# Optimization experiments

Hardware: AMD Instinct MI355X
Metric: run time of the kernel (lower is better)

## Reference

```python
import jax, jax.numpy as jnp
import numpy as np

B, T, A, F, K, DQ, DV = 64, 1024, 128, 1024, 31, 1024, 512  # filters F == T required by source math


def setup_inputs() -> dict:
    key = jax.random.key(0)
    ks = jax.random.split(key, 8)
    s = 0.05
    return {
        "query": jax.random.normal(ks[0], (B, 1, DQ), jnp.float32),
        "value": jax.random.normal(ks[1], (B, T, DV), jnp.float32),
        "attention_weights_cat": jax.random.uniform(ks[2], (B, T, 2), jnp.float32),
        "Wq": jax.random.normal(ks[3], (DQ, A), jnp.float32) * s,
        "Wm": jax.random.normal(ks[4], (DV, A), jnp.float32) * s,
        "Wv": jax.random.normal(ks[5], (A, 1), jnp.float32) * s,
        "Wconv": jax.random.normal(ks[6], (K, 2, F), jnp.float32) * s,
        "Wloc": jax.random.normal(ks[7], (T, A), jnp.float32) * s,
    }


def reference(query, value, attention_weights_cat, Wq, Wm, Wv, Wconv, Wloc):
    # query_layer: Dense(tanh, no bias): [B,1,DQ] -> [B,1,A]
    q = jnp.tanh(jnp.einsum('bld,da->bla', query, Wq))
    # memory_layer: Dense(tanh, no bias): [B,T,DV] -> [B,T,A]
    v = jnp.tanh(jnp.einsum('btd,da->bta', value, Wm))
    # location conv (SAME, no bias): [B,T,2] -> [B,T,F]
    loc = jax.lax.conv_general_dilated(
        attention_weights_cat, Wconv, window_strides=(1,), padding='SAME',
        dimension_numbers=('NWC', 'WIO', 'NWC'))
    # source transposes [0,2,1] then Dense(T->A, tanh): [B,F,T] -> [B,F,A]
    loc = jnp.tanh(jnp.einsum('bft,ta->bfa', jnp.transpose(loc, (0, 2, 1)), Wloc))
    # additive score (F == T so broadcast add is element-aligned): [B,T,1]
    score = jnp.einsum('bta,ao->bto', jnp.tanh(q + v + loc), Wv)
    alignment = jax.nn.softmax(score, axis=1)                # softmax over time
    context = jnp.sum(alignment * v, axis=1)                  # [B,A]
    return context, jnp.transpose(alignment, (0, 2, 1))       # [B,1,T]
```

## Files before the change

### kernel.cpp

```cpp
#include <hip/hip_runtime.h>
#include <hip/hip_bf16.h>

#define BB 64
#define TT 1024
#define AA 128
#define FF 1024
#define DQ 1024
#define DV 512

typedef __bf16 bf16x8_t __attribute__((ext_vector_type(8)));
typedef __bf16 bf16x4_t __attribute__((ext_vector_type(4)));
typedef float f32x4_t __attribute__((ext_vector_type(4)));
typedef _Float16 f16x4_t __attribute__((ext_vector_type(4)));

__device__ __forceinline__ float ftanh(float x) {
    float e = __expf(2.0f * x);
    return 1.0f - 2.0f / (e + 1.0f);
}

__device__ __forceinline__ __bf16 bhi(float x) { return (__bf16)x; }
__device__ __forceinline__ __bf16 blo(float x) {
    __bf16 h = (__bf16)x;
    return (__bf16)(x - (float)h);
}

__global__ __launch_bounds__(256) void k_prep(
    const float* __restrict__ Wm, const float* __restrict__ Wconv,
    const float* __restrict__ Wloc, const float* __restrict__ query,
    const float* __restrict__ Wq,
    __bf16* __restrict__ pwmhi, __bf16* __restrict__ pwmlo,
    __bf16* __restrict__ wcthi, __bf16* __restrict__ wctlo,
    __bf16* __restrict__ pwlhi, __bf16* __restrict__ pwllo,
    float* __restrict__ q_ws) {
    __shared__ float ls[128 * 65];
    int bx = blockIdx.x, tid = threadIdx.x;
    if (bx < 16) {
        int s = bx, d0 = s * 32;
        for (int i = tid; i < 4096; i += 256) {
            int dd = i >> 7, a = i & 127;
            ls[a * 33 + dd] = Wm[(d0 + dd) * AA + a];
        }
        __syncthreads();
#pragma unroll
        for (int u = 0; u < 2; u++) {
            int pos = tid * 2 + u;
            int l15 = pos & 15, lq = (pos >> 4) & 3, g = pos >> 6;
            bf16x8_t h8, l8;
#pragma unroll
            for (int j = 0; j < 8; j++) {
                float x = ls[(g * 16 + l15) * 33 + lq * 8 + j];
                h8[j] = bhi(x);
                l8[j] = blo(x);
            }
            size_t off = (size_t)(s * 512 + pos) * 8;
            *(bf16x8_t*)(pwmhi + off) = h8;
            *(bf16x8_t*)(pwmlo + off) = l8;
        }
    } else if (bx < 24) {
        int f0 = (bx - 16) * 128;
        for (int i = tid; i < 8192; i += 256) {
            int kc = i >> 7, f = i & 127;
            ls[f * 65 + kc] = (kc < 62) ? Wconv[kc * FF + f0 + f] : 0.f;
        }
        __syncthreads();
        int f = tid >> 1, half = tid & 1;
#pragma unroll
        for (int g = 0; g < 4; g++) {
            bf16x8_t h8, l8;
#pragma unroll
            for (int j = 0; j < 8; j++) {
                float x = ls[f * 65 + half * 32 + g * 8 + j];
                h8[j] = bhi(x);
                l8[j] = blo(x);
            }
            size_t off = (size_t)(f0 + f) * 64 + half * 32 + g * 8;
            *(bf16x8_t*)(wcthi + off) = h8;
            *(bf16x8_t*)(wctlo + off) = l8;
        }
    } else if (bx < 56) {
        int s2 = bx - 24, t0 = s2 * 32;
        for (int i = tid; i < 4096; i += 256) {
            int tt = i >> 7, a = i & 127;
            ls[a * 33 + tt] = Wloc[(t0 + tt) * AA + a];
        }
        __syncthreads();
#pragma unroll
        for (int u = 0; u < 2; u++) {
            int pos = tid * 2 + u;
            int l15 = pos & 15, lq = (pos >> 4) & 3, g = pos >> 6;
            bf16x8_t h8, l8;
#pragma unroll
            for (int j = 0; j < 8; j++) {
                float x = ls[(g * 16 + l15) * 33 + lq * 8 + j];
                h8[j] = bhi(x);
                l8[j] = blo(x);
            }
            size_t off = (size_t)(s2 * 512 + pos) * 8;
            *(bf16x8_t*)(pwlhi + off) = h8;
            *(bf16x8_t*)(pwllo + off) = l8;
        }
    } else {
        int b = bx - 56;
        int a = tid & 127, half = tid >> 7;
        const float* qrow = query + b * DQ + half * 512;
        float a0 = 0.f, a1 = 0.f, a2 = 0.f, a3 = 0.f;
        for (int d = 0; d < 512; d += 4) {
            float4 qv = *(const float4*)(qrow + d);
            int dg = (half * 512 + d) * AA + a;
            a0 += qv.x * Wq[dg];
            a1 += qv.y * Wq[dg + AA];
            a2 += qv.z * Wq[dg + 2 * AA];
            a3 += qv.w * Wq[dg + 3 * AA];
        }
        ls[tid] = a0 + a1 + a2 + a3;
        __syncthreads();
        if (half == 0) q_ws[b * AA + a] = ftanh(ls[a] + ls[a + 128]);
    }
}

__global__ __launch_bounds__(256) void k_zq(
    const float* __restrict__ xcat,
    const __bf16* __restrict__ pwlhi, const __bf16* __restrict__ pwllo,
    float* __restrict__ ztf) {
    int bx = blockIdx.x;
    int b = bx & 63, ahh = (bx >> 6) & 1, kh = bx >> 7;
    int tid = threadIdx.x;
    __shared__ float xs0[1056], xs1[1056];
    __shared__ float zs[64 * 66];
    for (int i = tid; i < 1056; i += 256) {
        int t = i - 16;
        float2 xv = (t >= 0 && t < TT) ? *(const float2*)(xcat + (size_t)(b * TT + t) * 2)
                                       : make_float2(0.f, 0.f);
        xs0[i] = xv.x;
        xs1[i] = xv.y;
    }
    __syncthreads();
    int lane = tid & 63, wid = tid >> 6;
    int wm = wid >> 1, wn = wid & 1;
    int l15 = lane & 15, lq = lane >> 4;

    f32x4_t zacc[2][2];
#pragma unroll
    for (int mi = 0; mi < 2; mi++)
#pragma unroll
        for (int ni = 0; ni < 2; ni++) zacc[mi][ni] = (f32x4_t){0.f, 0.f, 0.f, 0.f};

    int phase = bx & 15;
    for (int sl = 0; sl < 16; sl++) {
        int s = kh * 16 + ((sl + phase) & 15);
        int t0 = s * 32;
        bf16x8_t bh[2], bl[2];
#pragma unroll
        for (int ni = 0; ni < 2; ni++) {
            int g = ahh * 4 + wn * 2 + ni;
            size_t poff = (size_t)((s * 8 + g) * 64 + lane) * 8;
            bh[ni] = *(const bf16x8_t*)(pwlhi + poff);
            bl[ni] = *(const bf16x8_t*)(pwllo + poff);
        }
        bf16x8_t ah_[2], al_[2];
#pragma unroll
        for (int mi = 0; mi < 2; mi++) {
            int kc = wm * 32 + mi * 16 + l15;
            const float* xsc = (kc & 1) ? xs1 : xs0;
            int base = t0 + lq * 8 + (kc >> 1) + 1;
#pragma unroll
            for (int j = 0; j < 8; j++) {
                float x = xsc[base + j];
                ah_[mi][j] = bhi(x);
                al_[mi][j] = blo(x);
            }
        }
#pragma unroll
        for (int ni = 0; ni < 2; ni++)
#pragma unroll
            for (int mi = 0; mi < 2; mi++) {
                zacc[mi][ni] = __builtin_amdgcn_mfma_f32_16x16x32_bf16(ah_[mi], bh[ni], zacc[mi][ni], 0, 0, 0);
                zacc[mi][ni] = __builtin_amdgcn_mfma_f32_16x16x32_bf16(al_[mi], bh[ni], zacc[mi][ni], 0, 0, 0);
                zacc[mi][ni] = __builtin_amdgcn_mfma_f32_16x16x32_bf16(ah_[mi], bl[ni], zacc[mi][ni], 0, 0, 0);
            }
    }
#pragma unroll
    for (int mi = 0; mi < 2; mi++)
#pragma unroll
        for (int ni = 0; ni < 2; ni++)
#pragma unroll
            for (int r = 0; r < 4; r++)
                zs[(wm * 32 + mi * 16 + lq * 4 + r) * 66 + wn * 32 + ni * 16 + l15] = zacc[mi][ni][r];
    __syncthreads();
    int a_local = tid & 63, seg = tid >> 6;
#pragma unroll
    for (int g = 0; g < 2; g++) {
        f32x4_t v0, v1;
#pragma unroll
        for (int j = 0; j < 4; j++) {
            v0[j] = zs[(seg * 16 + g * 8 + j) * 66 + a_local];
            v1[j] = zs[(seg * 16 + g * 8 + 4 + j) * 66 + a_local];
        }
        float* dst = ztf + (size_t)kh * 524288 +
                     ((size_t)b * AA + ahh * 64 + a_local) * 64 + seg * 16 + g * 8;
        *(f32x4_t*)dst = v0;
        *(f32x4_t*)(dst + 4) = v1;
    }
}

__global__ __launch_bounds__(256, 2) void k_main(
    const float* __restrict__ value,
    const __bf16* __restrict__ pwmhi, const __bf16* __restrict__ pwmlo,
    const __bf16* __restrict__ wcthi, const __bf16* __restrict__ wctlo,
    const float* __restrict__ ztf,
    const float* __restrict__ q_ws, const float* __restrict__ Wv,
    _Float16* __restrict__ v_ws, float* __restrict__ score) {
    int b = blockIdx.x >> 3;
    int trow0 = (blockIdx.x & 7) << 7;
    int tid = threadIdx.x;
    int lane = tid & 63, wid = tid >> 6;
    int wm = wid >> 1, wn = wid & 1;
    int l15 = lane & 15, lq = lane >> 4;
    int phase = (blockIdx.x + (blockIdx.x >> 3)) & 15;

    __shared__ __align__(16) float As[2][128 * 32];
    __shared__ float sc_red[256];

    f32x4_t acc[4][4];
#pragma unroll
    for (int mi = 0; mi < 4; mi++)
#pragma unroll
        for (int ni = 0; ni < 4; ni++) acc[mi][ni] = (f32x4_t){0.f, 0.f, 0.f, 0.f};

    int l3 = lane >> 3;
    int su = (lane & 7) ^ l3;
    const float* aG[4];
    unsigned aL[4];
#pragma unroll
    for (int i = 0; i < 4; i++) {
        int row = (wid * 4 + i) * 8 + l3;
        aG[i] = value + (size_t)(b * TT + trow0 + row) * DV + su * 4;
        aL[i] = (unsigned)((wid * 4 + i) * 1024);
    }
    const __bf16* pbh0 = pwmhi + (size_t)(wn * 256 + lane) * 8;
    const __bf16* pbl0 = pwmlo + (size_t)(wn * 256 + lane) * 8;

    bf16x8_t bhb[2][4], blb[2][4];

#define GL4(dst, ptr, OFF) \
    asm volatile("global_load_dwordx4 %0, %1, off offset:" OFF : "=v"(dst) : "v"(ptr))
#define ISSUE_B(bf, s) { \
    const __bf16* _bh = pbh0 + (size_t)(s) * 4096; \
    const __bf16* _bl = pbl0 + (size_t)(s) * 4096; \
    GL4(bhb[bf][0], _bh, "0"); \
    GL4(bhb[bf][1], _bh, "1024"); \
    GL4(bhb[bf][2], _bh, "2048"); \
    GL4(bhb[bf][3], _bh, "3072"); \
    GL4(blb[bf][0], _bl, "0"); \
    GL4(blb[bf][1], _bl, "1024"); \
    GL4(blb[bf][2], _bl, "2048"); \
    GL4(blb[bf][3], _bl, "3072"); }
#define STAGE_A(bf, s)                                                                      \
    {                                                                                       \
        _Pragma("unroll") for (int i = 0; i < 4; i++)                                       \
            __builtin_amdgcn_global_load_lds(                                               \
                (const __attribute__((address_space(1))) void*)(aG[i] + (s) * 32),          \
                (__attribute__((address_space(3))) void*)((char*)&As[bf][0] + aL[i]),       \
                16, 0, 0);                                                                  \
    }

    {
        int s0 = phase & 15;
        ISSUE_B(0, s0);
        STAGE_A(0, s0);
    }

    int swz = l15 & 7;
#pragma unroll
    for (int it = 0; it < 16; ++it) {
        const int cb = it & 1;
        __syncthreads();
        __builtin_amdgcn_sched_barrier(0);

        bf16x8_t ah[4], al[4];
#pragma unroll
        for (int mi = 0; mi < 4; mi++) {
            int row = wm * 64 + mi * 16 + l15;
            const char* rbase = (const char*)&As[cb][0] + row * 128;
            f32x4_t f0 = *(const f32x4_t*)(rbase + (((lq * 2 + 0) ^ swz) << 4));
            f32x4_t f1 = *(const f32x4_t*)(rbase + (((lq * 2 + 1) ^ swz) << 4));
#pragma unroll
            for (int j = 0; j < 4; j++) {
                ah[mi][j] = bhi(f0[j]);
                al[mi][j] = blo(f0[j]);
                ah[mi][4 + j] = bhi(f1[j]);
                al[mi][4 + j] = blo(f1[j]);
            }
        }
        if (it < 15) {
            const int s = (it + 1 + phase) & 15;
            ISSUE_B(cb ^ 1, s);
            STAGE_A(cb ^ 1, s);
        }
#pragma unroll
        for (int mi = 0; mi < 4; mi++)
#pragma unroll
            for (int ni = 0; ni < 4; ni++) {
                acc[mi][ni] = __builtin_amdgcn_mfma_f32_16x16x32_bf16(ah[mi], bhb[cb][ni], acc[mi][ni], 0, 0, 0);
                acc[mi][ni] = __builtin_amdgcn_mfma_f32_16x16x32_bf16(al[mi], bhb[cb][ni], acc[mi][ni], 0, 0, 0);
                acc[mi][ni] = __builtin_amdgcn_mfma_f32_16x16x32_bf16(ah[mi], blb[cb][ni], acc[mi][ni], 0, 0, 0);
            }
    }
#undef ISSUE_B
#undef STAGE_A
#undef GL4

    f32x4_t lacc[4][4];
#pragma unroll
    for (int mi = 0; mi < 4; mi++)
#pragma unroll
        for (int ni = 0; ni < 4; ni++) lacc[mi][ni] = (f32x4_t){0.f, 0.f, 0.f, 0.f};
#pragma unroll
    for (int kc0 = 0; kc0 < 64; kc0 += 32) {
        bf16x8_t a2h[4], a2l[4], b2h[4], b2l[4];
#pragma unroll
        for (int mi = 0; mi < 4; mi++) {
            int f = trow0 + wm * 64 + mi * 16 + l15;
            a2h[mi] = *(const bf16x8_t*)(wcthi + (size_t)f * 64 + kc0 + lq * 8);
            a2l[mi] = *(const bf16x8_t*)(wctlo + (size_t)f * 64 + kc0 + lq * 8);
        }
#pragma unroll
        for (int ni = 0; ni < 4; ni++) {
            int a = wn * 64 + ni * 16 + l15;
            const float* zp = ztf + ((size_t)b * AA + a) * 64 + kc0 + lq * 8;
            f32x4_t z0 = *(const f32x4_t*)zp + *(const f32x4_t*)(zp + 524288);
            f32x4_t z1 = *(const f32x4_t*)(zp + 4) + *(const f32x4_t*)(zp + 524292);
#pragma unroll
            for (int j = 0; j < 4; j++) {
                b2h[ni][j] = bhi(z0[j]);
                b2l[ni][j] = blo(z0[j]);
                b2h[ni][4 + j] = bhi(z1[j]);
                b2l[ni][4 + j] = blo(z1[j]);
            }
        }
#pragma unroll
        for (int mi = 0; mi < 4; mi++)
#pragma unroll
            for (int ni = 0; ni < 4; ni++) {
                lacc[mi][ni] = __builtin_amdgcn_mfma_f32_16x16x32_bf16(a2h[mi], b2h[ni], lacc[mi][ni], 0, 0, 0);
                lacc[mi][ni] = __builtin_amdgcn_mfma_f32_16x16x32_bf16(a2l[mi], b2h[ni], lacc[mi][ni], 0, 0, 0);
                lacc[mi][ni] = __builtin_amdgcn_mfma_f32_16x16x32_bf16(a2h[mi], b2l[ni], lacc[mi][ni], 0, 0, 0);
            }
    }

    float qv[4], wv[4];
#pragma unroll
    for (int ni = 0; ni < 4; ni++) {
        int a = wn * 64 + ni * 16 + l15;
        qv[ni] = q_ws[b * AA + a];
        wv[ni] = Wv[a];
    }
#pragma unroll
    for (int mi = 0; mi < 4; mi++) {
#pragma unroll
        for (int r = 0; r < 4; r++) {
            int tl = wm * 64 + mi * 16 + lq * 4 + r;
            int t = trow0 + tl;
            float s = 0.f;
#pragma unroll
            for (int ni = 0; ni < 4; ni++) {
                float v = ftanh(acc[mi][ni][r]);
                float loc = ftanh(lacc[mi][ni][r]);
                int a = wn * 64 + ni * 16 + l15;
                v_ws[(size_t)(b * TT + t) * AA + a] = (_Float16)v;
                s += ftanh(qv[ni] + v + loc) * wv[ni];
            }
            s += __shfl_xor(s, 1, 64);
            s += __shfl_xor(s, 2, 64);
            s += __shfl_xor(s, 4, 64);
            s += __shfl_xor(s, 8, 64);
            if (l15 == 0) sc_red[wn * 128 + tl] = s;
        }
    }
    __syncthreads();
    if (tid < 128) score[b * TT + trow0 + tid] = sc_red[tid] + sc_red[128 + tid];
}

__global__ void k_softmax(const float* __restrict__ score, float* __restrict__ out_align,
                          float* __restrict__ out_ctx) {
    int b = blockIdx.x, tid = threadIdx.x;
    if (tid < 128) out_ctx[b * AA + tid] = 0.f;
    __shared__ float red[4];
    float s[4];
#pragma unroll
    for (int i = 0; i < 4; i++) s[i] = score[b * TT + tid + i * 256];
    float m = fmaxf(fmaxf(s[0], s[1]), fmaxf(s[2], s[3]));
    for (int off = 32; off; off >>= 1) m = fmaxf(m, __shfl_xor(m, off, 64));
    int wid = tid >> 6;
    if ((tid & 63) == 0) red[wid] = m;
    __syncthreads();
    float M = fmaxf(fmaxf(red[0], red[1]), fmaxf(red[2], red[3]));
    __syncthreads();
    float e[4];
    float sum = 0.f;
#pragma unroll
    for (int i = 0; i < 4; i++) { e[i] = __expf(s[i] - M); sum += e[i]; }
    for (int off = 32; off; off >>= 1) sum += __shfl_xor(sum, off, 64);
    if ((tid & 63) == 0) red[wid] = sum;
    __syncthreads();
    float inv = 1.0f / (red[0] + red[1] + red[2] + red[3]);
#pragma unroll
    for (int i = 0; i < 4; i++) out_align[b * TT + tid + i * 256] = e[i] * inv;
}

__global__ void k_context(const float* __restrict__ align, const _Float16* __restrict__ v_ws,
                          float* __restrict__ out_ctx) {
    int b = blockIdx.y, t0 = blockIdx.x * 64, tid = threadIdx.x;
    int a0 = (tid & 31) * 4, tl = tid >> 5;
    __shared__ float sh[8 * 132];
    f32x4_t acc = (f32x4_t){0.f, 0.f, 0.f, 0.f};
    for (int tt = tl; tt < 64; tt += 8) {
        float w = align[b * TT + t0 + tt];
        f16x4_t vv = *(const f16x4_t*)(v_ws + (size_t)(b * TT + t0 + tt) * AA + a0);
        acc[0] += w * (float)vv[0];
        acc[1] += w * (float)vv[1];
        acc[2] += w * (float)vv[2];
        acc[3] += w * (float)vv[3];
    }
    *(f32x4_t*)&sh[tl * 132 + a0] = acc;
    __syncthreads();
    if (tid < 128) {
        float s = 0.f;
#pragma unroll
        for (int j = 0; j < 8; j++) s += sh[j * 132 + tid];
        atomicAdd(out_ctx + b * AA + tid, s);
    }
}

extern "C" void kernel_launch(void* const* d_in, const int* in_sizes, int n_in,
                              void* d_out, int out_size, void* d_ws, size_t ws_size,
                              hipStream_t stream) {
    const float* query = (const float*)d_in[0];
    const float* value = (const float*)d_in[1];
    const float* xcat  = (const float*)d_in[2];
    const float* Wq    = (const float*)d_in[3];
    const float* Wm    = (const float*)d_in[4];
    const float* Wv    = (const float*)d_in[5];
    const float* Wconv = (const float*)d_in[6];
    const float* Wloc  = (const float*)d_in[7];
    float* out = (float*)d_out;

    float* ws = (float*)d_ws;
    float* q_ws  = ws;
    float* sc_ws = q_ws + 8192;
    _Float16* v_ws = (_Float16*)(sc_ws + 65536);
    __bf16* pwmhi = (__bf16*)(sc_ws + 65536 + 4194304);
    __bf16* pwmlo = pwmhi + 65536;
    __bf16* wcthi = pwmlo + 65536;
    __bf16* wctlo = wcthi + 65536;
    __bf16* pwlhi = wctlo + 65536;
    __bf16* pwllo = pwlhi + 131072;
    float* ztf = (float*)(pwllo + 131072);

    k_prep<<<120, 256, 0, stream>>>(Wm, Wconv, Wloc, query, Wq,
                                    pwmhi, pwmlo, wcthi, wctlo, pwlhi, pwllo, q_ws);
    k_zq<<<256, 256, 0, stream>>>(xcat, pwlhi, pwllo, ztf);
    k_main<<<512, 256, 0, stream>>>(value, pwmhi, pwmlo, wcthi, wctlo, ztf,
                                    q_ws, Wv, v_ws, sc_ws);
    k_softmax<<<BB, 256, 0, stream>>>(sc_ws, out + 8192, out);
    k_context<<<dim3(16, BB), 256, 0, stream>>>(out + 8192, v_ws, out);
}
```

Measured before the change: 269.0 us.

## Stage Wm hi/lo tiles through LDS with async loads and explicit waitcnt

Replaces the per-wave register prefetch of the split bf16 Wm fragments with global_load_lds staging into double-buffered shared tiles, so each block fetches B once instead of each wave pair fetching its own copy. The loop now issues the next stage before compute, waits with an explicit vmcnt, and uses raw s_barrier plus a trailing barrier instead of __syncthreads. The main loop is no longer unrolled. This cuts redundant global traffic and VGPRs for B, but adds LDS reads and footprint (which may hurt occupancy) and depends on hand-counted waitcnt values being correct.

```diff
diff --git a/kernel.cpp b/kernel.cpp
--- a/kernel.cpp
+++ b/kernel.cpp
@@ -219,6 +219,8 @@
     int phase = (blockIdx.x + (blockIdx.x >> 3)) & 15;
 
     __shared__ __align__(16) float As[2][128 * 32];
+    __shared__ __align__(16) __bf16 Bh[2][512 * 8];
+    __shared__ __align__(16) __bf16 Bl[2][512 * 8];
     __shared__ float sc_red[256];
 
     f32x4_t acc[4][4];
@@ -237,44 +239,48 @@
         aG[i] = value + (size_t)(b * TT + trow0 + row) * DV + su * 4;
         aL[i] = (unsigned)((wid * 4 + i) * 1024);
     }
-    const __bf16* pbh0 = pwmhi + (size_t)(wn * 256 + lane) * 8;
-    const __bf16* pbl0 = pwmlo + (size_t)(wn * 256 + lane) * 8;
-
-    bf16x8_t bhb[2][4], blb[2][4];
-
-#define GL4(dst, ptr, OFF) \
-    asm volatile("global_load_dwordx4 %0, %1, off offset:" OFF : "=v"(dst) : "v"(ptr))
-#define ISSUE_B(bf, s) { \
-    const __bf16* _bh = pbh0 + (size_t)(s) * 4096; \
-    const __bf16* _bl = pbl0 + (size_t)(s) * 4096; \
-    GL4(bhb[bf][0], _bh, "0"); \
-    GL4(bhb[bf][1], _bh, "1024"); \
-    GL4(bhb[bf][2], _bh, "2048"); \
-    GL4(bhb[bf][3], _bh, "3072"); \
-    GL4(blb[bf][0], _bl, "0"); \
-    GL4(blb[bf][1], _bl, "1024"); \
-    GL4(blb[bf][2], _bl, "2048"); \
-    GL4(blb[bf][3], _bl, "3072"); }
-#define STAGE_A(bf, s)                                                                      \
+    const __bf16* bGh[2];
+    const __bf16* bGl[2];
+    unsigned bL[2];
+#pragma unroll
+    for (int j = 0; j < 2; j++) {
+        int c = (wid * 2 + j) * 64 + lane;
+        bGh[j] = pwmhi + (size_t)c * 8;
+        bGl[j] = pwmlo + (size_t)c * 8;
+        bL[j] = (unsigned)((wid * 2 + j) * 1024);
+    }
+
+#define STAGE(bf, s)                                                                        \
     {                                                                                       \
         _Pragma("unroll") for (int i = 0; i < 4; i++)                                       \
             __builtin_amdgcn_global_load_lds(                                               \
-                (const __attribute__((address_space(1))) void*)(aG[i] + (s) * 32),          \
+                (const __attribute__((address_space(1))) void*)(aG[i] + (size_t)(s) * 32),  \
                 (__attribute__((address_space(3))) void*)((char*)&As[bf][0] + aL[i]),       \
                 16, 0, 0);                                                                  \
-    }
-
-    {
-        int s0 = phase & 15;
-        ISSUE_B(0, s0);
-        STAGE_A(0, s0);
-    }
+        _Pragma("unroll") for (int j = 0; j < 2; j++) {                                     \
+            __builtin_amdgcn_global_load_lds(                                               \
+                (const __attribute__((address_space(1))) void*)(bGh[j] + (size_t)(s) * 4096),\
+                (__attribute__((address_space(3))) void*)((char*)&Bh[bf][0] + bL[j]),       \
+                16, 0, 0);                                                                  \
+            __builtin_amdgcn_global_load_lds(                                               \
+                (const __attribute__((address_space(1))) void*)(bGl[j] + (size_t)(s) * 4096),\
+                (__attribute__((address_space(3))) void*)((char*)&Bl[bf][0] + bL[j]),       \
+                16, 0, 0);                                                                  \
+        }                                                                                   \
+    }
+
+    STAGE(0, phase);
 
     int swz = l15 & 7;
-#pragma unroll
     for (int it = 0; it < 16; ++it) {
-        const int cb = it & 1;
-        __syncthreads();
+        int cb = it & 1;
+        if (it < 15) {
+            STAGE(cb ^ 1, (it + 1 + phase) & 15);
+            asm volatile("s_waitcnt vmcnt(8)");
+        } else {
+            asm volatile("s_waitcnt vmcnt(0)");
+        }
+        __builtin_amdgcn_s_barrier();
         __builtin_amdgcn_sched_barrier(0);
 
         bf16x8_t ah[4], al[4];
@@ -292,23 +298,26 @@
                 al[mi][4 + j] = blo(f1[j]);
             }
         }
-        if (it < 15) {
-            const int s = (it + 1 + phase) & 15;
-            ISSUE_B(cb ^ 1, s);
-            STAGE_A(cb ^ 1, s);
+        bf16x8_t bh[4], bl[4];
+#pragma unroll
+        for (int ni = 0; ni < 4; ni++) {
+            int c = (wn * 4 + ni) * 64 + lane;
+            bh[ni] = *(const bf16x8_t*)(&Bh[cb][0] + (size_t)c * 8);
+            bl[ni] = *(const bf16x8_t*)(&Bl[cb][0] + (size_t)c * 8);
         }
 #pragma unroll
         for (int mi = 0; mi < 4; mi++)
 #pragma unroll
             for (int ni = 0; ni < 4; ni++) {
-                acc[mi][ni] = __builtin_amdgcn_mfma_f32_16x16x32_bf16(ah[mi], bhb[cb][ni], acc[mi][ni], 0, 0, 0);
-                acc[mi][ni] = __builtin_amdgcn_mfma_f32_16x16x32_bf16(al[mi], bhb[cb][ni], acc[mi][ni], 0, 0, 0);
-                acc[mi][ni] = __builtin_amdgcn_mfma_f32_16x16x32_bf16(ah[mi], blb[cb][ni], acc[mi][ni], 0, 0, 0);
-            }
-    }
-#undef ISSUE_B
-#undef STAGE_A
-#undef GL4
+                acc[mi][ni] = __builtin_amdgcn_mfma_f32_16x16x32_bf16(ah[mi], bh[ni], acc[mi][ni], 0, 0, 0);
+                acc[mi][ni] = __builtin_amdgcn_mfma_f32_16x16x32_bf16(al[mi], bh[ni], acc[mi][ni], 0, 0, 0);
+                acc[mi][ni] = __builtin_amdgcn_mfma_f32_16x16x32_bf16(ah[mi], bl[ni], acc[mi][ni], 0, 0, 0);
+            }
+        __builtin_amdgcn_sched_barrier(0);
+        asm volatile("s_waitcnt lgkmcnt(0)");
+        __builtin_amdgcn_s_barrier();
+    }
+#undef STAGE
 
     f32x4_t lacc[4][4];
 #pragma unroll
```

Measured after the change: 266.0 us. No clear change (-1.1%).
